# Performance work log

Hardware: AMD Instinct MI355X
Metric: run time of the kernel (lower is better)

The kernel has to match this reference:

```python
import jax, jax.numpy as jnp
import numpy as np

B, L, D = 4, 2048, 1024
H, DK, DV = 16, 64, 64


def setup_inputs() -> dict:
    key = jax.random.key(0)
    ks = jax.random.split(key, 11)
    s = 1.0 / np.sqrt(D)
    so = 1.0 / np.sqrt(H * DV)
    return {
        "query": jax.random.normal(ks[0], (B, L, D), jnp.float32),
        "key": jax.random.normal(ks[1], (B, L, D), jnp.float32),
        "value": jax.random.normal(ks[2], (B, L, D), jnp.float32),
        "W_q": jax.random.uniform(ks[3], (D, H * DK), jnp.float32, -s, s),
        "b_q": jax.random.uniform(ks[4], (H * DK,), jnp.float32, -s, s),
        "W_k": jax.random.uniform(ks[5], (D, H * DK), jnp.float32, -s, s),
        "b_k": jax.random.uniform(ks[6], (H * DK,), jnp.float32, -s, s),
        "W_v": jax.random.uniform(ks[7], (D, H * DV), jnp.float32, -s, s),
        "b_v": jax.random.uniform(ks[8], (H * DV,), jnp.float32, -s, s),
        "W_o": jax.random.uniform(ks[9], (H * DV, D), jnp.float32, -so, so),
        "b_o": jax.random.uniform(ks[10], (D,), jnp.float32, -so, so),
    }


def reference(query, key, value, W_q, b_q, W_k, b_k, W_v, b_v, W_o, b_o):
    # QKV projections, then split heads: [B, L, H*d] -> [B, H, L, d]
    q = (query @ W_q + b_q).reshape(B, L, H, DK).transpose(0, 2, 1, 3)
    k = (key @ W_k + b_k).reshape(B, L, H, DK).transpose(0, 2, 1, 3)
    v = (value @ W_v + b_v).reshape(B, L, H, DV).transpose(0, 2, 1, 3)
    # scaled dot-product attention: softmax(q k^T / sqrt(dk)) v
    scores = jnp.einsum("bhqd,bhkd->bhqk", q, k) / jnp.sqrt(jnp.float32(DK))
    attn = jax.nn.softmax(scores, axis=-1)
    ctx = jnp.einsum("bhqk,bhkd->bhqd", attn, v)
    # combine heads: [B, H, L, dv] -> [B, L, H*dv], output projection
    out = ctx.transpose(0, 2, 1, 3).reshape(B, L, H * DV) @ W_o + b_o
    return out
```

## Files before the change

### kernel.cpp

```cpp
#include <hip/hip_runtime.h>

#define BATCH 4
#define LSEQ 2048
#define DMODEL 1024
#define NHEAD 16
#define DHEAD 64
#define MTOT (BATCH * LSEQ)

typedef _Float16 f16;
typedef _Float16 f16x8 __attribute__((ext_vector_type(8)));
typedef _Float16 f16x4 __attribute__((ext_vector_type(4)));
typedef _Float16 f16x2 __attribute__((ext_vector_type(2)));
typedef float f32x4 __attribute__((ext_vector_type(4)));
typedef float f32x16 __attribute__((ext_vector_type(16)));
typedef unsigned int u32;
typedef unsigned int u32x4 __attribute__((ext_vector_type(4)));

#define SCORE_SCALE 0.180336878f

typedef const __attribute__((address_space(1))) void gvoid;
typedef __attribute__((address_space(3))) void lvoid;
#define GLDS16(g, l) __builtin_amdgcn_global_load_lds((gvoid*)(g), (lvoid*)(l), 16, 0, 0)

__global__ __launch_bounds__(256)
void cvt3_f32_f16(const float* __restrict__ in0, const float* __restrict__ in1,
                  const float* __restrict__ in2, f16* __restrict__ out, int n8)
{
    const int y = blockIdx.y;
    const float* in = (y == 0) ? in0 : (y == 1) ? in1 : in2;
    f16* o = out + (size_t)y * (size_t)n8 * 8;
    int i = blockIdx.x * 256 + threadIdx.x;
    if (i >= n8) return;
    float4 a = ((const float4*)in)[2 * i];
    float4 b = ((const float4*)in)[2 * i + 1];
    f16x8 v;
    v[0] = (f16)a.x; v[1] = (f16)a.y; v[2] = (f16)a.z; v[3] = (f16)a.w;
    v[4] = (f16)b.x; v[5] = (f16)b.y; v[6] = (f16)b.z; v[7] = (f16)b.w;
    ((f16x8*)o)[i] = v;
}

__global__ __launch_bounds__(256)
void wconv4(const float* __restrict__ W0, const float* __restrict__ W1,
            const float* __restrict__ W2, const float* __restrict__ W3,
            f16* __restrict__ WtBase)
{
    __shared__ float T[64][68];
    const int z = blockIdx.z;
    const float* W = (z == 0) ? W0 : (z == 1) ? W1 : (z == 2) ? W2 : W3;
    f16* Wt = WtBase + (size_t)z * DMODEL * DMODEL;
    const int t = threadIdx.x;
    const int k0 = blockIdx.y * 64, n0 = blockIdx.x * 64;
    const int tr = t >> 4, tc = (t & 15) * 4;
#pragma unroll
    for (int p = 0; p < 64; p += 16) {
        float4 v = *(const float4*)&W[(size_t)(k0 + tr + p) * DMODEL + n0 + tc];
        *(float4*)&T[tr + p][tc] = v;
    }
    __syncthreads();
    const int n = t >> 2, kc = (t & 3) * 16;
    f16x8 o0, o1;
#pragma unroll
    for (int j = 0; j < 8; ++j) o0[j] = (f16)T[kc + j][n];
#pragma unroll
    for (int j = 0; j < 8; ++j) o1[j] = (f16)T[kc + 8 + j][n];
    *(f16x8*)&Wt[(size_t)(n0 + n) * DMODEL + k0 + kc] = o0;
    *(f16x8*)&Wt[(size_t)(n0 + n) * DMODEL + k0 + kc + 8] = o1;
}

__global__ __launch_bounds__(256)
void gemm_f16(const f16* __restrict__ A, const f16* __restrict__ Bt,
              const float* __restrict__ b0, const float* __restrict__ b1,
              const float* __restrict__ b2, void* __restrict__ Cout, int fused)
{
    __shared__ f16 As2[2][128][32];
    __shared__ f16 Bs2[2][128][32];

    const int t = threadIdx.x;
    const int lane = t & 63, w = t >> 6;
    const int quad = lane >> 4, m16 = lane & 15;
    const int m0 = blockIdx.x * 128;
    const int n0 = blockIdx.y * 128;
    const int wm = (w & 1) * 64, wn = (w >> 1) * 64;

    const int which = fused ? (n0 >> 10) : 0;

    f32x4 acc[4][4] = {};

    const f16* Ag = A + (size_t)which * MTOT * DMODEL
                      + (size_t)(m0 + (t >> 2)) * DMODEL + (t & 3) * 8;
    const f16* Bg = Bt + (size_t)(n0 + (t >> 2)) * DMODEL + (t & 3) * 8;
    f16* Al = &As2[0][0][0] + t * 8;
    f16* Bl = &Bs2[0][0][0] + t * 8;

    for (int k0 = 0; k0 < DMODEL; k0 += 64) {
        __syncthreads();
#pragma unroll
        for (int h = 0; h < 2; ++h) {
            GLDS16(Ag + k0 + h * 32, Al + h * 4096);
            GLDS16(Ag + k0 + h * 32 + (size_t)64 * DMODEL, Al + h * 4096 + 2048);
            GLDS16(Bg + k0 + h * 32, Bl + h * 4096);
            GLDS16(Bg + k0 + h * 32 + (size_t)64 * DMODEL, Bl + h * 4096 + 2048);
        }
        __syncthreads();
#pragma unroll
        for (int h = 0; h < 2; ++h) {
            f16x8 af[4], bf[4];
#pragma unroll
            for (int mi = 0; mi < 4; ++mi)
                af[mi] = *(const f16x8*)&As2[h][wm + mi * 16 + m16][quad * 8];
#pragma unroll
            for (int ni = 0; ni < 4; ++ni)
                bf[ni] = *(const f16x8*)&Bs2[h][wn + ni * 16 + m16][quad * 8];
#pragma unroll
            for (int mi = 0; mi < 4; ++mi)
#pragma unroll
                for (int ni = 0; ni < 4; ++ni)
                    acc[mi][ni] = __builtin_amdgcn_mfma_f32_16x16x32_f16(
                        af[mi], bf[ni], acc[mi][ni], 0, 0, 0);
        }
    }

    if (fused) {
        const float* bp = (which == 0) ? b0 : (which == 1) ? b1 : b2;
        const float scale = (which == 0) ? SCORE_SCALE : 1.0f;
        f16* o = (f16*)Cout + (size_t)which * MTOT * DMODEL;
#pragma unroll
        for (int ni = 0; ni < 4; ++ni) {
            const int nn = (n0 + wn + ni * 16 + m16) & 1023;
            const float bv = bp[nn];
            const int h = nn >> 6, d = nn & 63;
#pragma unroll
            for (int mi = 0; mi < 4; ++mi) {
                const int mrow = m0 + wm + mi * 16 + quad * 4;
                const int b = mrow >> 11, l0 = mrow & (LSEQ - 1);
                if (which < 2) {
#pragma unroll
                    for (int j = 0; j < 4; ++j) {
                        const float v = (acc[mi][ni][j] + bv) * scale;
                        o[(((size_t)(b * NHEAD + h) * LSEQ + l0 + j) << 6) + d] = (f16)v;
                    }
                } else {
                    f16x4 pk;
#pragma unroll
                    for (int j = 0; j < 4; ++j) pk[j] = (f16)(acc[mi][ni][j] + bv);
                    *(f16x4*)&o[(((size_t)(b * NHEAD + h) << 6) + d) * LSEQ + l0] = pk;
                }
            }
        }
    } else {
#pragma unroll
        for (int ni = 0; ni < 4; ++ni) {
            const int n = n0 + wn + ni * 16 + m16;
            const float bv = b0[n];
#pragma unroll
            for (int mi = 0; mi < 4; ++mi)
#pragma unroll
                for (int j = 0; j < 4; ++j) {
                    const int m = m0 + wm + mi * 16 + quad * 4 + j;
                    ((float*)Cout)[(size_t)m * DMODEL + n] = acc[mi][ni][j] + bv;
                }
        }
    }
}

__global__ __launch_bounds__(512, 4)
void attn_mfma(const f16* __restrict__ Qh, const f16* __restrict__ Kh,
               const f16* __restrict__ Vt, f16* __restrict__ ctx)
{
    __shared__ f16 Ks[2][64 * 64];
    __shared__ f16 Vs[2][64 * 64];

    const int t = threadIdx.x;
    const int lane = t & 63, w = t >> 6;
    const int l31 = lane & 31;
    const int hi = lane >> 5;
    const int swz = (l31 & 7) << 4;

    const int bid = blockIdx.x;
    const int x = bid & 7, rest = bid >> 3;
    const int qt = rest & 7;
    const int g = x + 8 * (rest >> 3);
    const int q0 = qt * 256 + w * 32;

    const f16* Qg = Qh + (size_t)g * LSEQ * DHEAD;
    const f16* Kg = Kh + (size_t)g * LSEQ * DHEAD;
    const f16* Vg = Vt + (size_t)g * LSEQ * DHEAD;

    f16x8 qf[4];
#pragma unroll
    for (int s = 0; s < 4; ++s)
        qf[s] = *(const f16x8*)&Qg[(size_t)(q0 + l31) * DHEAD + 16 * s + 8 * hi];

    const int srow = t >> 3;
    const int sxs = ((t & 7) << 4) ^ ((srow & 7) << 4);
    const f16* ksrc = Kg + (size_t)srow * DHEAD + (sxs >> 1);
    const f16* vsrc = Vg + (size_t)srow * LSEQ + (sxs >> 1);
    f16* kdst0 = &Ks[0][0] + t * 8;
    f16* vdst0 = &Vs[0][0] + t * 8;
    f16* kdst1 = &Ks[1][0] + t * 8;
    f16* vdst1 = &Vs[1][0] + t * 8;

    f32x16 ctxa[2] = {};
    float lsum = 0.f;

    GLDS16(ksrc, kdst0);
    GLDS16(vsrc, vdst0);
    __syncthreads();

    auto proc = [&](const f32x16& stv, const int kb, const char* Vc) {
        u32 d[8];
#pragma unroll
        for (int r = 0; r < 8; ++r) {
            const float p0 = __builtin_amdgcn_exp2f(stv[2 * r]);
            const float p1 = __builtin_amdgcn_exp2f(stv[2 * r + 1]);
            lsum += p0 + p1;
            f16x2 pk; pk[0] = (f16)p0; pk[1] = (f16)p1;
            d[r] = __builtin_bit_cast(u32, pk);
        }
#pragma unroll
        for (int s = 0; s < 2; ++s) {
            const u32 sendE = hi ? d[4 * s + 0] : d[4 * s + 2];
            const u32 sendO = hi ? d[4 * s + 1] : d[4 * s + 3];
            const u32 recvE = __shfl_xor(sendE, 32);
            const u32 recvO = __shfl_xor(sendO, 32);
            u32x4 paw;
            paw[0] = hi ? recvE : d[4 * s + 0];
            paw[1] = hi ? recvO : d[4 * s + 1];
            paw[2] = hi ? d[4 * s + 2] : recvE;
            paw[3] = hi ? d[4 * s + 3] : recvO;
            const f16x8 pa = __builtin_bit_cast(f16x8, paw);
            const int kbyte = kb * 64 + 32 * s + 16 * hi;
#pragma unroll
            for (int d32 = 0; d32 < 2; ++d32) {
                const int vrow = d32 * 32 + l31;
                const f16x8 vf = *(const f16x8*)(Vc + vrow * 128 + (kbyte ^ swz));
                ctxa[d32] = __builtin_amdgcn_mfma_f32_32x32x16_f16(
                    pa, vf, ctxa[d32], 0, 0, 0);
            }
        }
    };

    auto compute = [&](const f16* Kbuf, const f16* Vbuf) {
        const char* Kc = (const char*)Kbuf;
        const char* Vc = (const char*)Vbuf;
        f32x16 s0 = {}, s1 = {};
#pragma unroll
        for (int s = 0; s < 4; ++s) {
            const int cb = 32 * s + 16 * hi;
            const f16x8 kf0 = *(const f16x8*)(Kc + l31 * 128 + (cb ^ swz));
            const f16x8 kf1 = *(const f16x8*)(Kc + (l31 + 32) * 128 + (cb ^ swz));
            s0 = __builtin_amdgcn_mfma_f32_32x32x16_f16(kf0, qf[s], s0, 0, 0, 0);
            s1 = __builtin_amdgcn_mfma_f32_32x32x16_f16(kf1, qf[s], s1, 0, 0, 0);
        }
        proc(s0, 0, Vc);
        proc(s1, 1, Vc);
    };

    for (int kt = 0; kt < LSEQ; kt += 128) {
        if (kt + 64 < LSEQ) {
            GLDS16(ksrc + (size_t)(kt + 64) * DHEAD, kdst1);
            GLDS16(vsrc + (kt + 64), vdst1);
        }
        compute(&Ks[0][0], &Vs[0][0]);
        __syncthreads();
        if (kt + 128 < LSEQ) {
            GLDS16(ksrc + (size_t)(kt + 128) * DHEAD, kdst0);
            GLDS16(vsrc + (kt + 128), vdst0);
        }
        compute(&Ks[1][0], &Vs[1][0]);
        __syncthreads();
    }

    const float l = lsum + __shfl_xor(lsum, 32);
    const float linv = 1.0f / l;
    const int batch = g >> 4, h = g & 15;
#pragma unroll
    for (int r = 0; r < 16; ++r) {
        const int qr = (r & 3) + 8 * (r >> 2) + 4 * hi;
        const float inv = __shfl(linv, qr);
        f16* op = ctx + ((size_t)(batch * LSEQ + q0 + qr)) * DMODEL
                      + h * 64 + l31;
        op[0]  = (f16)(ctxa[0][r] * inv);
        op[32] = (f16)(ctxa[1][r] * inv);
    }
}

extern "C" void kernel_launch(void* const* d_in, const int* in_sizes, int n_in,
                              void* d_out, int out_size, void* d_ws, size_t ws_size,
                              hipStream_t stream)
{
    const float* query = (const float*)d_in[0];
    const float* key   = (const float*)d_in[1];
    const float* value = (const float*)d_in[2];
    const float* W_q   = (const float*)d_in[3];
    const float* b_q   = (const float*)d_in[4];
    const float* W_k   = (const float*)d_in[5];
    const float* b_k   = (const float*)d_in[6];
    const float* W_v   = (const float*)d_in[7];
    const float* b_v   = (const float*)d_in[8];
    const float* W_o   = (const float*)d_in[9];
    const float* b_o   = (const float*)d_in[10];
    float* out = (float*)d_out;

    const size_t MAT = (size_t)MTOT * DMODEL;
    f16* base = (f16*)d_ws;
    f16* Aq   = base;
    f16* Qhp  = base + 3 * MAT;
    f16* ctxh = base + 6 * MAT;
    f16* Wtq  = base + 7 * MAT;
    f16* Wto  = Wtq + (size_t)3 * DMODEL * DMODEL;

    const int n8 = (int)(MAT / 8);
    cvt3_f32_f16<<<dim3(n8 / 256, 3), 256, 0, stream>>>(query, key, value, Aq, n8);
    wconv4<<<dim3(DMODEL / 64, DMODEL / 64, 4), 256, 0, stream>>>(W_q, W_k, W_v, W_o, Wtq);

    gemm_f16<<<dim3(MTOT / 128, 3 * DMODEL / 128), 256, 0, stream>>>(
        Aq, Wtq, b_q, b_k, b_v, Qhp, 1);

    attn_mfma<<<BATCH * NHEAD * (LSEQ / 256), 512, 0, stream>>>(
        Qhp, Qhp + MAT, Qhp + 2 * MAT, ctxh);

    gemm_f16<<<dim3(MTOT / 128, DMODEL / 128), 256, 0, stream>>>(
        ctxh, Wto, b_o, nullptr, nullptr, out, 0);
}
```

Baseline: 337.8 us.

## Replace QKV projection GEMM with 256x256-tile 8-phase pipelined MFMA kernel

Adds a new QKV GEMM kernel that uses 256x256 output tiles, 512 threads and 64-deep K steps. Operand tiles are streamed into swizzled double-buffered LDS via global_load_lds, and each K pair is split into eight phases that interleave LDS reads, async global loads and 16x16x32 MFMA bursts, using explicit waitcnt, barriers and setprio. The aim is to raise arithmetic intensity and hide memory latency behind compute in the largest GEMM. In exchange it needs large LDS and register use per block and fragile hand-tuned wait counts. The epilogue also writes V in a transposed layout, which the attention kernel must expect.

Result: slower. 348.5 us (+3.2%).

```diff
diff --git a/kernel.cpp b/kernel.cpp
--- a/kernel.cpp
+++ b/kernel.cpp
@@ -21,6 +21,10 @@
 typedef const __attribute__((address_space(1))) void gvoid;
 typedef __attribute__((address_space(3))) void lvoid;
 #define GLDS16(g, l) __builtin_amdgcn_global_load_lds((gvoid*)(g), (lvoid*)(l), 16, 0, 0)
+
+#define WAITCNT(s) do { asm volatile("s_waitcnt " s ::: "memory"); \
+                        __builtin_amdgcn_sched_barrier(0); } while (0)
+#define BAR() __builtin_amdgcn_s_barrier()
 
 __global__ __launch_bounds__(256)
 void cvt3_f32_f16(const float* __restrict__ in0, const float* __restrict__ in1,
@@ -65,6 +69,171 @@
     for (int j = 0; j < 8; ++j) o1[j] = (f16)T[kc + 8 + j][n];
     *(f16x8*)&Wt[(size_t)(n0 + n) * DMODEL + k0 + kc] = o0;
     *(f16x8*)&Wt[(size_t)(n0 + n) * DMODEL + k0 + kc + 8] = o1;
+}
+
+__global__ __launch_bounds__(512, 2)
+void gemm_qkv_8ph(const f16* __restrict__ A, const f16* __restrict__ Bt,
+                  const float* __restrict__ b0, const float* __restrict__ b1,
+                  const float* __restrict__ b2, f16* __restrict__ Cout)
+{
+    __shared__ f16 As[2][2][128][64];
+    __shared__ f16 Bs[2][2][128][64];
+
+    const int t = threadIdx.x;
+    const int lane = t & 63;
+    const int w = t >> 6, wr = w >> 2, wc = w & 3;
+    const int quad = lane >> 4, m16 = lane & 15;
+    const int m0 = blockIdx.x * 256, n0 = blockIdx.y * 256;
+    const int which = n0 >> 10;
+
+    const int sr = t >> 3;
+    const int sc = ((t & 7) << 4) ^ ((sr & 7) << 4);
+    const f16* Asrc = A + (size_t)which * MTOT * DMODEL
+                        + (size_t)(m0 + sr) * DMODEL + (sc >> 1);
+    const f16* Bsrc = Bt + (size_t)(n0 + sr) * DMODEL + (sc >> 1);
+
+    auto stA = [&](int buf, int h, int kt) {
+        const f16* s = Asrc + (size_t)(h * 128) * DMODEL + kt * 64;
+        GLDS16(s,               &As[buf][h][0][0] + t * 8);
+        GLDS16(s + 64 * DMODEL, &As[buf][h][64][0] + t * 8);
+    };
+    auto stB = [&](int buf, int h, int kt) {
+        const f16* s = Bsrc + (size_t)(h * 128) * DMODEL + kt * 64;
+        GLDS16(s,               &Bs[buf][h][0][0] + t * 8);
+        GLDS16(s + 64 * DMODEL, &Bs[buf][h][64][0] + t * 8);
+    };
+
+    const int fsw = (m16 & 7) << 4;
+    auto rdA = [&](int buf, int mf, int ks) -> f16x8 {
+        return *(const f16x8*)((const char*)&As[buf][wr][0][0]
+                               + (mf * 16 + m16) * 128
+                               + ((ks * 64 + quad * 16) ^ fsw));
+    };
+    auto rdB = [&](int buf, int nf, int ks) -> f16x8 {
+        return *(const f16x8*)((const char*)&Bs[buf][wc >> 1][0][0]
+                               + ((wc & 1) * 64 + nf * 16 + m16) * 128
+                               + ((ks * 64 + quad * 16) ^ fsw));
+    };
+
+    f32x4 acc[8][4] = {};
+    f16x8 af[4][2], bf[4][2];
+
+    auto ldA = [&](int buf, int mg) {
+#pragma unroll
+        for (int mi = 0; mi < 4; ++mi)
+#pragma unroll
+            for (int ks = 0; ks < 2; ++ks)
+                af[mi][ks] = rdA(buf, mg * 4 + mi, ks);
+    };
+    auto ldB = [&](int buf) {
+#pragma unroll
+        for (int nf = 0; nf < 4; ++nf)
+#pragma unroll
+            for (int ks = 0; ks < 2; ++ks)
+                bf[nf][ks] = rdB(buf, nf, ks);
+    };
+    auto mfma16 = [&](int mg, int np) {
+        __builtin_amdgcn_s_setprio(1);
+#pragma unroll
+        for (int mi = 0; mi < 4; ++mi)
+#pragma unroll
+            for (int ni = 0; ni < 2; ++ni)
+#pragma unroll
+                for (int ks = 0; ks < 2; ++ks)
+                    acc[mg * 4 + mi][np * 2 + ni] =
+                        __builtin_amdgcn_mfma_f32_16x16x32_f16(
+                            af[mi][ks], bf[np * 2 + ni][ks],
+                            acc[mg * 4 + mi][np * 2 + ni], 0, 0, 0);
+        __builtin_amdgcn_s_setprio(0);
+    };
+
+    stB(0, 0, 0); stB(0, 1, 0); stA(0, 0, 0); stA(0, 1, 0);
+    stB(1, 0, 1); stB(1, 1, 1); stA(1, 0, 1);
+    WAITCNT("vmcnt(6)");
+    BAR();
+    __builtin_amdgcn_sched_barrier(0);
+
+    const int NHI = (DMODEL / 128) - 1;
+    for (int i = 0; i < NHI; ++i) {
+        const int T1 = 2 * i + 1, T2 = 2 * i + 2, T3 = 2 * i + 3;
+        ldA(0, 0); ldB(0);
+        stA(1, 1, T1);
+        BAR(); WAITCNT("lgkmcnt(0)");
+        mfma16(0, 0);
+        BAR(); __builtin_amdgcn_sched_barrier(0);
+        stB(0, 0, T2);
+        BAR(); WAITCNT("lgkmcnt(0)");
+        mfma16(0, 1);
+        BAR(); __builtin_amdgcn_sched_barrier(0);
+        ldA(0, 1);
+        stB(0, 1, T2);
+        BAR(); WAITCNT("lgkmcnt(0)");
+        mfma16(1, 0);
+        BAR(); __builtin_amdgcn_sched_barrier(0);
+        stA(0, 0, T2);
+        WAITCNT("vmcnt(6)");
+        BAR(); WAITCNT("lgkmcnt(0)");
+        mfma16(1, 1);
+        BAR(); __builtin_amdgcn_sched_barrier(0);
+        ldA(1, 0); ldB(1);
+        stA(0, 1, T2);
+        BAR(); WAITCNT("lgkmcnt(0)");
+        mfma16(0, 0);
+        BAR(); __builtin_amdgcn_sched_barrier(0);
+        stB(1, 0, T3);
+        BAR(); WAITCNT("lgkmcnt(0)");
+        mfma16(0, 1);
+        BAR(); __builtin_amdgcn_sched_barrier(0);
+        ldA(1, 1);
+        stB(1, 1, T3);
+        BAR(); WAITCNT("lgkmcnt(0)");
+        mfma16(1, 0);
+        BAR(); __builtin_amdgcn_sched_barrier(0);
+        stA(1, 0, T3);
+        WAITCNT("vmcnt(6)");
+        BAR(); WAITCNT("lgkmcnt(0)");
+        mfma16(1, 1);
+        BAR(); __builtin_amdgcn_sched_barrier(0);
+    }
+
+    stA(1, 1, 2 * NHI + 1);
+    WAITCNT("vmcnt(0)");
+    BAR();
+    ldA(0, 0); ldB(0); WAITCNT("lgkmcnt(0)");
+    mfma16(0, 0); mfma16(0, 1);
+    ldA(0, 1); WAITCNT("lgkmcnt(0)");
+    mfma16(1, 0); mfma16(1, 1);
+    ldA(1, 0); ldB(1); WAITCNT("lgkmcnt(0)");
+    mfma16(0, 0); mfma16(0, 1);
+    ldA(1, 1); WAITCNT("lgkmcnt(0)");
+    mfma16(1, 0); mfma16(1, 1);
+
+    const float* bp = (which == 0) ? b0 : (which == 1) ? b1 : b2;
+    const float scale = (which == 0) ? SCORE_SCALE : 1.0f;
+    f16* o = Cout + (size_t)which * MTOT * DMODEL;
+#pragma unroll
+    for (int nf = 0; nf < 4; ++nf) {
+        const int nn = (n0 + wc * 64 + nf * 16 + m16) & 1023;
+        const float bv = bp[nn];
+        const int h = nn >> 6, d = nn & 63;
+#pragma unroll
+        for (int mf = 0; mf < 8; ++mf) {
+            const int mrow = m0 + wr * 128 + mf * 16 + quad * 4;
+            const int b = mrow >> 11, l0 = mrow & (LSEQ - 1);
+            if (which < 2) {
+#pragma unroll
+                for (int j = 0; j < 4; ++j) {
+                    const float v = (acc[mf][nf][j] + bv) * scale;
+                    o[(((size_t)(b * NHEAD + h) * LSEQ + l0 + j) << 6) + d] = (f16)v;
+                }
+            } else {
+                f16x4 pk;
+#pragma unroll
+                for (int j = 0; j < 4; ++j) pk[j] = (f16)(acc[mf][nf][j] + bv);
+                *(f16x4*)&o[(((size_t)(b * NHEAD + h) << 6) + d) * LSEQ + l0] = pk;
+            }
+        }
+    }
 }
 
 __global__ __launch_bounds__(256)
@@ -314,8 +483,8 @@
     cvt3_f32_f16<<<dim3(n8 / 256, 3), 256, 0, stream>>>(query, key, value, Aq, n8);
     wconv4<<<dim3(DMODEL / 64, DMODEL / 64, 4), 256, 0, stream>>>(W_q, W_k, W_v, W_o, Wtq);
 
-    gemm_f16<<<dim3(MTOT / 128, 3 * DMODEL / 128), 256, 0, stream>>>(
-        Aq, Wtq, b_q, b_k, b_v, Qhp, 1);
+    gemm_qkv_8ph<<<dim3(MTOT / 256, 3 * DMODEL / 256), 512, 0, stream>>>(
+        Aq, Wtq, b_q, b_k, b_v, Qhp);
 
     attn_mfma<<<BATCH * NHEAD * (LSEQ / 256), 512, 0, stream>>>(
         Qhp, Qhp + MAT, Qhp + 2 * MAT, ctxh);
```
